# Kernel optimization log

Measured on AMD Instinct MI355X. Metric: run time of the kernel, lower is better.

The kernel has to match this reference:

```python
import jax, jax.numpy as jnp
import numpy as np

NUM_CLASSES = 10
OUTPUT_DIM = 128
HIDDEN_DIM = 64


def setup_inputs() -> dict:
    key = jax.random.key(0)
    k1, k2, k3, k4, k5, k6 = jax.random.split(key, 6)
    B, S, F = 16, 4096, 512
    X_support = jax.random.normal(k1, (B, S, F), dtype=jnp.float32)
    y_support = jax.random.randint(k2, (B, S), 0, NUM_CLASSES, dtype=jnp.int32)
    # MLP params: Linear(6, HIDDEN) -> GELU -> Linear(HIDDEN, OUTPUT)
    w1 = jax.random.normal(k3, (6, HIDDEN_DIM), dtype=jnp.float32) * (1.0 / np.sqrt(6.0))
    b1 = jax.random.normal(k4, (HIDDEN_DIM,), dtype=jnp.float32) * 0.01
    w2 = jax.random.normal(k5, (HIDDEN_DIM, OUTPUT_DIM), dtype=jnp.float32) * (1.0 / np.sqrt(HIDDEN_DIM))
    b2 = jax.random.normal(k6, (OUTPUT_DIM,), dtype=jnp.float32) * 0.01
    return {"X_support": X_support, "y_support": y_support,
            "w1": w1, "b1": b1, "w2": w2, "b2": b2}


def _feature_target_stats(X, y):
    """Vectorized equivalent of FeatureTargetStatsEncoder per-(batch,feature) loops.
    X: [B, S, F] float, y: [B, S] int class labels. Returns stats [B, F, 6]."""
    B, S, F = X.shape
    missing_rate = jnp.isnan(X).astype(X.dtype).mean(axis=1)           # [B, F]
    Xc = jnp.nan_to_num(X, nan=0.0)
    gmean = Xc.mean(axis=1)                                            # [B, F]
    variance = Xc.var(axis=1)                                          # biased (unbiased=False)
    absX = jnp.abs(Xc)
    mean_abs = absX.mean(axis=1)
    max_abs = absX.max(axis=1)
    # unique_ratio: count distinct values per (b, f) via sort + diff
    xs = jnp.sort(Xc, axis=1)
    n_unique = 1.0 + (jnp.diff(xs, axis=1) != 0).astype(Xc.dtype).sum(axis=1)
    unique_ratio = n_unique / S
    # classification target score: between-class variance / overall variance
    onehot = jax.nn.one_hot(y, NUM_CLASSES, dtype=Xc.dtype)            # [B, S, C]
    counts = onehot.sum(axis=1)                                        # [B, C]
    csum = jnp.einsum('bsc,bsf->bcf', onehot, Xc)                      # [B, C, F]
    cmean = csum / jnp.maximum(counts, 1.0)[:, :, None]
    dev2 = (cmean - gmean[:, None, :]) ** 2
    between = (counts[:, :, None] * dev2).sum(axis=1) / jnp.maximum(counts.sum(axis=1), 1.0)[:, None]
    target_score = between / jnp.maximum(variance, 1e-6)
    stats = jnp.stack([target_score, missing_rate, unique_ratio,
                       variance, mean_abs, max_abs], axis=-1)          # [B, F, 6]
    return jnp.nan_to_num(stats, nan=0.0, posinf=0.0, neginf=0.0)


def reference(X_support, y_support, w1, b1, w2, b2):
    stats = _feature_target_stats(X_support, y_support)                # [B, F, 6]
    h = jax.nn.gelu(stats @ w1 + b1, approximate=False)               # exact GELU like nn.GELU()
    return h @ w2 + b2                                                 # [B, F, OUTPUT_DIM]
```

## Files before the change

kernel.cpp:

```cpp
#include <hip/hip_runtime.h>
#include <math.h>

#define NS 4096
#define NF 512
#define NB 16
#define NC 10
#define HSIZE 8192
#define HMASK 8191
#define HEMPTY 0xFFFFFFFFu
#define WS_XT_OFF 1024

__global__ void count_classes_kernel(const int* __restrict__ y, float* __restrict__ counts) {
    __shared__ int hist[NC];
    const int b = blockIdx.x;
    if (threadIdx.x < NC) hist[threadIdx.x] = 0;
    __syncthreads();
    for (int s = threadIdx.x; s < NS; s += blockDim.x)
        atomicAdd(&hist[y[b * NS + s]], 1);
    __syncthreads();
    if (threadIdx.x < NC) counts[b * NC + threadIdx.x] = (float)hist[threadIdx.x];
}

__device__ __forceinline__ float wave_reduce_add(float v) {
    #pragma unroll
    for (int off = 32; off > 0; off >>= 1) v += __shfl_down(v, off, 64);
    return v;
}
__device__ __forceinline__ float wave_reduce_max(float v) {
    #pragma unroll
    for (int off = 32; off > 0; off >>= 1) v = fmaxf(v, __shfl_down(v, off, 64));
    return v;
}

__device__ __forceinline__ unsigned int pat_of(float x) {
    if (x != x) x = 0.f;
    unsigned int p = __float_as_uint(x);
    return (p == 0x80000000u) ? 0u : p;
}

__device__ __forceinline__ float resolve1(unsigned int* hash,
                                          unsigned int s, unsigned int p, unsigned int o) {
    if (o == HEMPTY) return 1.f;
    if (o == p)      return 0.f;
    for (;;) {
        s = (s + 1) & HMASK;
        const unsigned int oo = atomicCAS(&hash[s], HEMPTY, p);
        if (oo == HEMPTY) return 1.f;
        if (oo == p)      return 0.f;
    }
}

__device__ __forceinline__ float hash8(unsigned int* hash, const float4 u, const float4 v) {
    const unsigned int p0 = pat_of(u.x), p1 = pat_of(u.y), p2 = pat_of(u.z), p3 = pat_of(u.w);
    const unsigned int p4 = pat_of(v.x), p5 = pat_of(v.y), p6 = pat_of(v.z), p7 = pat_of(v.w);
    const unsigned int s0 = (p0 * 2654435761u) >> 19, s1 = (p1 * 2654435761u) >> 19;
    const unsigned int s2 = (p2 * 2654435761u) >> 19, s3 = (p3 * 2654435761u) >> 19;
    const unsigned int s4 = (p4 * 2654435761u) >> 19, s5 = (p5 * 2654435761u) >> 19;
    const unsigned int s6 = (p6 * 2654435761u) >> 19, s7 = (p7 * 2654435761u) >> 19;
    const unsigned int o0 = atomicCAS(&hash[s0], HEMPTY, p0);
    const unsigned int o1 = atomicCAS(&hash[s1], HEMPTY, p1);
    const unsigned int o2 = atomicCAS(&hash[s2], HEMPTY, p2);
    const unsigned int o3 = atomicCAS(&hash[s3], HEMPTY, p3);
    const unsigned int o4 = atomicCAS(&hash[s4], HEMPTY, p4);
    const unsigned int o5 = atomicCAS(&hash[s5], HEMPTY, p5);
    const unsigned int o6 = atomicCAS(&hash[s6], HEMPTY, p6);
    const unsigned int o7 = atomicCAS(&hash[s7], HEMPTY, p7);
    float u8 = 0.f;
    u8 += resolve1(hash, s0, p0, o0);
    u8 += resolve1(hash, s1, p1, o1);
    u8 += resolve1(hash, s2, p2, o2);
    u8 += resolve1(hash, s3, p3, o3);
    u8 += resolve1(hash, s4, p4, o4);
    u8 += resolve1(hash, s5, p5, o5);
    u8 += resolve1(hash, s6, p6, o6);
    u8 += resolve1(hash, s7, p7, o7);
    return u8;
}

__launch_bounds__(256)
__global__ void transpose_kernel(const float* __restrict__ X, float* __restrict__ XT,
                                 const int* __restrict__ y, float* __restrict__ counts) {
    __shared__ float t[64][65];
    __shared__ int hist[NC];
    const int b  = blockIdx.x;
    const int s0 = blockIdx.y * 64;
    const int f0 = blockIdx.z * 64;
    const int tid = threadIdx.x;

    const int fi = (tid & 15) * 4;
    const int si = tid >> 4;
    const float* Xb = X + ((size_t)b * NS + s0) * NF + f0;
    #pragma unroll
    for (int i = 0; i < 4; i++) {
        const int s = si + 16 * i;
        const float4 v = *(const float4*)(Xb + (size_t)s * NF + fi);
        t[s][fi + 0] = v.x; t[s][fi + 1] = v.y;
        t[s][fi + 2] = v.z; t[s][fi + 3] = v.w;
    }
    __syncthreads();

    const int sj = (tid & 15) * 4;
    const int fj = tid >> 4;
    float* XTb = XT + ((size_t)b * NF + f0) * NS + s0;
    #pragma unroll
    for (int i = 0; i < 4; i++) {
        const int f = fj + 16 * i;
        float4 v;
        v.x = t[sj + 0][f]; v.y = t[sj + 1][f];
        v.z = t[sj + 2][f]; v.w = t[sj + 3][f];
        *(float4*)(XTb + (size_t)f * NS + sj) = v;
    }

    if (blockIdx.y == 0 && blockIdx.z == 0) {
        if (tid < NC) hist[tid] = 0;
        __syncthreads();
        const int4* yb = (const int4*)(y + (size_t)b * NS);
        #pragma unroll
        for (int i = 0; i < 4; i++) {
            const int4 v = yb[i * 256 + tid];
            atomicAdd(&hist[v.x], 1); atomicAdd(&hist[v.y], 1);
            atomicAdd(&hist[v.z], 1); atomicAdd(&hist[v.w], 1);
        }
        __syncthreads();
        if (tid < NC) counts[b * NC + tid] = (float)hist[tid];
    }
}

__launch_bounds__(512, 8)
__global__ void fused_stats_mlp_xt(const float* __restrict__ XT,
                                   const int* __restrict__ y,
                                   const float* __restrict__ counts,
                                   const float* __restrict__ w1,
                                   const float* __restrict__ b1,
                                   const float* __restrict__ w2,
                                   const float* __restrict__ b2,
                                   float* __restrict__ out) {
    __shared__ __align__(16) unsigned int hash[HSIZE];

    const int w = blockIdx.x;
    const int g = (w & 7) * 1024 + (w >> 3);
    const int b = g >> 9;
    const int f = g & (NF - 1);
    const int tid = threadIdx.x;
    const int wave = tid >> 6;

    uint4* h4 = (uint4*)hash;
    const uint4 e4 = make_uint4(HEMPTY, HEMPTY, HEMPTY, HEMPTY);
    #pragma unroll
    for (int i = 0; i < HSIZE / 4 / 512; i++) h4[i * 512 + tid] = e4;
    __syncthreads();

    const float4* Xc4 = (const float4*)(XT + ((size_t)b * NF + f) * NS);
    const int4*   yp4 = (const int4*)(y + (size_t)b * NS);

    float sum = 0.f, sumsq = 0.f, sumabs = 0.f, maxabs = 0.f, nancnt = 0.f, uniq = 0.f;
    float csum[NC];
    #pragma unroll
    for (int c = 0; c < NC; c++) csum[c] = 0.f;

    if (wave < 4) {
        const int ts = tid;
        float4 xv[4]; int4 yv[4];
        #pragma unroll
        for (int k = 0; k < 4; k++) {
            xv[k] = Xc4[k * 256 + ts];
            yv[k] = yp4[k * 256 + ts];
        }
        #pragma unroll
        for (int k = 0; k < 4; k++) {
            const float xe[4] = { xv[k].x, xv[k].y, xv[k].z, xv[k].w };
            const int   ye[4] = { yv[k].x, yv[k].y, yv[k].z, yv[k].w };
            #pragma unroll
            for (int j = 0; j < 4; j++) {
                float x = xe[j];
                if (x != x) { nancnt += 1.f; x = 0.f; }
                sum += x;
                sumsq = fmaf(x, x, sumsq);
                const float a = fabsf(x);
                sumabs += a;
                maxabs = fmaxf(maxabs, a);
                const int yc = ye[j];
                #pragma unroll
                for (int c = 0; c < NC; c++) csum[c] += (yc == c) ? x : 0.f;
            }
        }
    } else {
        const int th = tid - 256;
        const float4 xa = Xc4[th];
        const float4 xb = Xc4[256 + th];
        const float4 xc = Xc4[512 + th];
        const float4 xd = Xc4[768 + th];
        uniq += hash8(hash, xa, xb);
        uniq += hash8(hash, xc, xd);
    }

    __syncthreads();

    float* r2 = (float*)hash;
    {
        float v16[16] = { sum, sumsq, sumabs, nancnt, uniq, maxabs,
                          csum[0], csum[1], csum[2], csum[3], csum[4],
                          csum[5], csum[6], csum[7], csum[8], csum[9] };
        #pragma unroll
        for (int c = 0; c < 16; c++) r2[c * 512 + tid] = v16[c];
    }
    __syncthreads();

    const int rc = tid >> 5;
    const int rq = tid & 31;
    float part = 0.f;
    #pragma unroll
    for (int j = 0; j < 16; j++) {
        const float v = r2[rc * 512 + rq + 32 * j];
        part = (rc == 5) ? fmaxf(part, v) : part + v;
    }
    #pragma unroll
    for (int off = 16; off > 0; off >>= 1) {
        const float o = __shfl_down(part, off, 32);
        part = (rc == 5) ? fmaxf(part, o) : part + o;
    }
    __syncthreads();
    if (rq == 0) r2[rc] = part;
    __syncthreads();

    float* stats_s = r2 + 32;
    float* h_s     = r2 + 64;

    if (tid == 0) {
        float t[16];
        #pragma unroll
        for (int v = 0; v < 16; v++) t[v] = r2[v];
        const float invS = 1.f / (float)NS;
        const float gmean    = t[0] * invS;
        const float variance = fmaxf(t[1] * invS - gmean * gmean, 0.f);
        const float mean_abs = t[2] * invS;
        const float missing  = t[3] * invS;
        const float n_unique = t[4];
        const float max_abs  = t[5];
        float between = 0.f;
        #pragma unroll
        for (int c = 0; c < NC; c++) {
            const float cnt = counts[b * NC + c];
            const float cm  = t[6 + c] / fmaxf(cnt, 1.f);
            const float d   = cm - gmean;
            between = fmaf(cnt * d, d, between);
        }
        between *= invS;
        const float target = between / fmaxf(variance, 1e-6f);
        float st[6] = { target, missing, n_unique * invS, variance, mean_abs, max_abs };
        #pragma unroll
        for (int i = 0; i < 6; i++) {
            float v = st[i];
            if (!(fabsf(v) < INFINITY)) v = 0.f;
            stats_s[i] = v;
        }
    }
    __syncthreads();

    if (tid < 64) {
        float z = b1[tid];
        #pragma unroll
        for (int i = 0; i < 6; i++) z = fmaf(stats_s[i], w1[i * 64 + tid], z);
        h_s[tid] = 0.5f * z * (1.f + erff(z * 0.70710678118654752440f));
    }
    __syncthreads();
    if (tid < 128) {
        float o = b2[tid];
        #pragma unroll
        for (int j = 0; j < 64; j++) o = fmaf(h_s[j], w2[j * 128 + tid], o);
        out[(size_t)g * 128 + tid] = o;
    }
}

__launch_bounds__(256)
__global__ void fused_stats_mlp_kernel(const float* __restrict__ X,
                                       const int* __restrict__ y,
                                       const float* __restrict__ counts,
                                       const float* __restrict__ w1,
                                       const float* __restrict__ b1,
                                       const float* __restrict__ w2,
                                       const float* __restrict__ b2,
                                       float* __restrict__ out) {
    __shared__ unsigned int hash[HSIZE];
    __shared__ float red[4][16];
    __shared__ float stats_s[6];
    __shared__ float h_s[64];

    const int w = blockIdx.x;
    const int g = (w & 7) * 1024 + (w >> 3);
    const int b = g >> 9;
    const int f = g & (NF - 1);
    const int tid = threadIdx.x;

    #pragma unroll
    for (int i = 0; i < HSIZE / 256; i++) hash[tid + i * 256] = HEMPTY;
    __syncthreads();

    const float* Xp = X + (size_t)b * NS * NF + f;
    const int*   yp = y + b * NS;

    float sum = 0.f, sumsq = 0.f, sumabs = 0.f, maxabs = 0.f, nancnt = 0.f, uniq = 0.f;
    float csum[NC];
    #pragma unroll
    for (int c = 0; c < NC; c++) csum[c] = 0.f;

    #pragma unroll
    for (int k0 = 0; k0 < 16; k0 += 8) {
        float xv[8]; int yv[8];
        #pragma unroll
        for (int k = 0; k < 8; k++) {
            const int s = (k0 + k) * 256 + tid;
            xv[k] = Xp[(size_t)s * NF];
            yv[k] = yp[s];
        }
        #pragma unroll
        for (int k = 0; k < 8; k++) {
            float x = xv[k];
            if (x != x) { nancnt += 1.f; x = 0.f; }
            sum += x;
            sumsq = fmaf(x, x, sumsq);
            const float a = fabsf(x);
            sumabs += a;
            maxabs = fmaxf(maxabs, a);
            const int yc = yv[k];
            #pragma unroll
            for (int c = 0; c < NC; c++) csum[c] += (yc == c) ? x : 0.f;
            unsigned int pat = __float_as_uint(x);
            if (pat == 0x80000000u) pat = 0u;
            unsigned int slot = (pat * 2654435761u) >> 19;
            for (;;) {
                const unsigned int old = atomicCAS(&hash[slot], HEMPTY, pat);
                if (old == HEMPTY) { uniq += 1.f; break; }
                if (old == pat) break;
                slot = (slot + 1) & HMASK;
            }
        }
    }

    sum    = wave_reduce_add(sum);
    sumsq  = wave_reduce_add(sumsq);
    sumabs = wave_reduce_add(sumabs);
    nancnt = wave_reduce_add(nancnt);
    uniq   = wave_reduce_add(uniq);
    maxabs = wave_reduce_max(maxabs);
    #pragma unroll
    for (int c = 0; c < NC; c++) csum[c] = wave_reduce_add(csum[c]);

    const int wave = tid >> 6, lane = tid & 63;
    if (lane == 0) {
        red[wave][0] = sum;    red[wave][1] = sumsq; red[wave][2] = sumabs;
        red[wave][3] = nancnt; red[wave][4] = uniq;  red[wave][5] = maxabs;
        #pragma unroll
        for (int c = 0; c < NC; c++) red[wave][6 + c] = csum[c];
    }
    __syncthreads();

    if (tid == 0) {
        float t[16];
        #pragma unroll
        for (int v = 0; v < 16; v++) t[v] = red[0][v];
        #pragma unroll
        for (int wv = 1; wv < 4; wv++) {
            #pragma unroll
            for (int v = 0; v < 16; v++) {
                if (v == 5) t[v] = fmaxf(t[v], red[wv][v]);
                else        t[v] += red[wv][v];
            }
        }
        const float invS = 1.f / (float)NS;
        const float gmean    = t[0] * invS;
        const float variance = fmaxf(t[1] * invS - gmean * gmean, 0.f);
        const float mean_abs = t[2] * invS;
        const float missing  = t[3] * invS;
        const float n_unique = t[4];
        const float max_abs  = t[5];
        float between = 0.f;
        #pragma unroll
        for (int c = 0; c < NC; c++) {
            const float cnt = counts[b * NC + c];
            const float cm  = t[6 + c] / fmaxf(cnt, 1.f);
            const float d   = cm - gmean;
            between += cnt * d * d;
        }
        between *= invS;
        const float target = between / fmaxf(variance, 1e-6f);
        float st[6] = { target, missing, n_unique * invS, variance, mean_abs, max_abs };
        #pragma unroll
        for (int i = 0; i < 6; i++) {
            float v = st[i];
            if (!(fabsf(v) < INFINITY)) v = 0.f;
            stats_s[i] = v;
        }
    }
    __syncthreads();

    if (tid < 64) {
        float z = b1[tid];
        #pragma unroll
        for (int i = 0; i < 6; i++) z = fmaf(stats_s[i], w1[i * 64 + tid], z);
        h_s[tid] = 0.5f * z * (1.f + erff(z * 0.70710678118654752440f));
    }
    __syncthreads();
    if (tid < 128) {
        float o = b2[tid];
        #pragma unroll
        for (int j = 0; j < 64; j++) o = fmaf(h_s[j], w2[j * 128 + tid], o);
        out[(size_t)g * 128 + tid] = o;
    }
}

extern "C" void kernel_launch(void* const* d_in, const int* in_sizes, int n_in,
                              void* d_out, int out_size, void* d_ws, size_t ws_size,
                              hipStream_t stream) {
    const float* X  = (const float*)d_in[0];
    const int*   y  = (const int*)d_in[1];
    const float* w1 = (const float*)d_in[2];
    const float* b1 = (const float*)d_in[3];
    const float* w2 = (const float*)d_in[4];
    const float* b2 = (const float*)d_in[5];
    float* out    = (float*)d_out;
    float* counts = (float*)d_ws;

    const size_t xt_bytes = (size_t)NB * NF * NS * sizeof(float);
    if (ws_size >= xt_bytes + WS_XT_OFF) {
        float* XT = (float*)((char*)d_ws + WS_XT_OFF);
        transpose_kernel<<<dim3(NB, NS / 64, NF / 64), 256, 0, stream>>>(X, XT, y, counts);
        fused_stats_mlp_xt<<<NB * NF, 512, 0, stream>>>(XT, y, counts, w1, b1, w2, b2, out);
    } else {
        count_classes_kernel<<<NB, 256, 0, stream>>>(y, counts);
        fused_stats_mlp_kernel<<<NB * NF, 256, 0, stream>>>(X, y, counts, w1, b1, w2, b2, out);
    }
}
```

Before: 348.6 us.

## Fuse moment and class-sum statistics into a striped transpose kernel

The transpose kernel now walks full sample columns in 16-feature stripes. While it writes the transposed copy, it also accumulates sum, sumsq, abs, max, NaN count and per-class sums, and stores the partials to a workspace buffer. The second kernel then only builds the hash for unique counting and runs the MLP, with all 512 threads doing hash work and no second reduction over moments. The grid shrinks to NB*NF/16 blocks with a serial loop over 32 sample tiles, which lowers parallelism in the transpose pass. The intent is to stop re-reading XT and y for the moments.

```diff
diff --git a/kernel.cpp b/kernel.cpp
--- a/kernel.cpp
+++ b/kernel.cpp
@@ -8,18 +8,10 @@
 #define HSIZE 8192
 #define HMASK 8191
 #define HEMPTY 0xFFFFFFFFu
-#define WS_XT_OFF 1024
-
-__global__ void count_classes_kernel(const int* __restrict__ y, float* __restrict__ counts) {
-    __shared__ int hist[NC];
-    const int b = blockIdx.x;
-    if (threadIdx.x < NC) hist[threadIdx.x] = 0;
-    __syncthreads();
-    for (int s = threadIdx.x; s < NS; s += blockDim.x)
-        atomicAdd(&hist[y[b * NS + s]], 1);
-    __syncthreads();
-    if (threadIdx.x < NC) counts[b * NC + threadIdx.x] = (float)hist[threadIdx.x];
-}
+#define TSR 128
+#define TSC 16
+#define WS_P_OFF  1024
+#define WS_XT_OFF (1024 + NB * NF * 16 * 4)
 
 __device__ __forceinline__ float wave_reduce_add(float v) {
     #pragma unroll
@@ -77,64 +69,103 @@
     return u8;
 }
 
-__launch_bounds__(256)
-__global__ void transpose_kernel(const float* __restrict__ X, float* __restrict__ XT,
-                                 const int* __restrict__ y, float* __restrict__ counts) {
-    __shared__ float t[64][65];
+__launch_bounds__(512, 4)
+__global__ void stripe_stats_kernel(const float* __restrict__ X,
+                                    float* __restrict__ XT,
+                                    const int* __restrict__ y,
+                                    float* __restrict__ P,
+                                    float* __restrict__ counts) {
+    __shared__ float t[TSR][TSC + 1];
+    __shared__ int ys[TSR];
     __shared__ int hist[NC];
-    const int b  = blockIdx.x;
-    const int s0 = blockIdx.y * 64;
-    const int f0 = blockIdx.z * 64;
+    const int b   = blockIdx.x;
+    const int f0  = blockIdx.y * TSC;
     const int tid = threadIdx.x;
-
-    const int fi = (tid & 15) * 4;
-    const int si = tid >> 4;
-    const float* Xb = X + ((size_t)b * NS + s0) * NF + f0;
-    #pragma unroll
-    for (int i = 0; i < 4; i++) {
-        const int s = si + 16 * i;
-        const float4 v = *(const float4*)(Xb + (size_t)s * NF + fi);
-        t[s][fi + 0] = v.x; t[s][fi + 1] = v.y;
-        t[s][fi + 2] = v.z; t[s][fi + 3] = v.w;
-    }
-    __syncthreads();
-
-    const int sj = (tid & 15) * 4;
-    const int fj = tid >> 4;
-    float* XTb = XT + ((size_t)b * NF + f0) * NS + s0;
-    #pragma unroll
-    for (int i = 0; i < 4; i++) {
-        const int f = fj + 16 * i;
-        float4 v;
-        v.x = t[sj + 0][f]; v.y = t[sj + 1][f];
-        v.z = t[sj + 2][f]; v.w = t[sj + 3][f];
-        *(float4*)(XTb + (size_t)f * NS + sj) = v;
-    }
-
-    if (blockIdx.y == 0 && blockIdx.z == 0) {
-        if (tid < NC) hist[tid] = 0;
+    const bool do_hist = (blockIdx.y == 0);
+    if (do_hist && tid < NC) hist[tid] = 0;
+
+    const int lrow = tid >> 2, lq = tid & 3;
+    const int col  = tid >> 5, rq = tid & 31;
+
+    const float* Xb = X + (size_t)b * NS * NF + f0 + lq * 4;
+    const int*   yb = y + (size_t)b * NS;
+
+    float sum = 0.f, sumsq = 0.f, sumabs = 0.f, maxabs = 0.f, nancnt = 0.f;
+    float csum[NC];
+    #pragma unroll
+    for (int c = 0; c < NC; c++) csum[c] = 0.f;
+
+    float4 xcur = *(const float4*)(Xb + (size_t)lrow * NF);
+    int4 ycur = make_int4(0, 0, 0, 0);
+    if (tid < TSR / 4) ycur = *(const int4*)(yb + tid * 4);
+
+    for (int it = 0; it < NS / TSR; ++it) {
+        const int s0 = it * TSR;
+        float4 xnext = xcur; int4 ynext = ycur;
+        if (it + 1 < NS / TSR) {
+            xnext = *(const float4*)(Xb + (size_t)(s0 + TSR + lrow) * NF);
+            if (tid < TSR / 4) ynext = *(const int4*)(yb + s0 + TSR + tid * 4);
+        }
         __syncthreads();
-        const int4* yb = (const int4*)(y + (size_t)b * NS);
-        #pragma unroll
-        for (int i = 0; i < 4; i++) {
-            const int4 v = yb[i * 256 + tid];
-            atomicAdd(&hist[v.x], 1); atomicAdd(&hist[v.y], 1);
-            atomicAdd(&hist[v.z], 1); atomicAdd(&hist[v.w], 1);
-        }
+        t[lrow][lq * 4 + 0] = xcur.x; t[lrow][lq * 4 + 1] = xcur.y;
+        t[lrow][lq * 4 + 2] = xcur.z; t[lrow][lq * 4 + 3] = xcur.w;
+        if (tid < TSR / 4) {
+            ys[tid * 4 + 0] = ycur.x; ys[tid * 4 + 1] = ycur.y;
+            ys[tid * 4 + 2] = ycur.z; ys[tid * 4 + 3] = ycur.w;
+        }
+        __syncthreads();
+        if (do_hist && tid < TSR) atomicAdd(&hist[ys[tid]], 1);
+
+        #pragma unroll
+        for (int j = 0; j < 4; j++) {
+            const int r = rq + 32 * j;
+            float x = t[r][col];
+            const int yc = ys[r];
+            if (x != x) { nancnt += 1.f; x = 0.f; }
+            sum += x;
+            sumsq = fmaf(x, x, sumsq);
+            const float a = fabsf(x);
+            sumabs += a;
+            maxabs = fmaxf(maxabs, a);
+            #pragma unroll
+            for (int c = 0; c < NC; c++) csum[c] += (yc == c) ? x : 0.f;
+        }
+        float4 wv;
+        wv.x = t[rq * 4 + 0][col]; wv.y = t[rq * 4 + 1][col];
+        wv.z = t[rq * 4 + 2][col]; wv.w = t[rq * 4 + 3][col];
+        *(float4*)(XT + ((size_t)b * NF + f0 + col) * NS + s0 + rq * 4) = wv;
+
+        xcur = xnext; ycur = ynext;
+    }
+
+    float st[16] = { sum, sumsq, sumabs, nancnt, maxabs,
+                     csum[0], csum[1], csum[2], csum[3], csum[4],
+                     csum[5], csum[6], csum[7], csum[8], csum[9], 0.f };
+    #pragma unroll
+    for (int s = 0; s < 15; s++) {
+        float v = st[s];
+        #pragma unroll
+        for (int off = 16; off > 0; off >>= 1) {
+            const float o = __shfl_down(v, off, 32);
+            v = (s == 4) ? fmaxf(v, o) : v + o;
+        }
+        if (rq == 0) P[((size_t)b * NF + f0 + col) * 16 + s] = v;
+    }
+    if (do_hist) {
         __syncthreads();
         if (tid < NC) counts[b * NC + tid] = (float)hist[tid];
     }
 }
 
 __launch_bounds__(512, 8)
-__global__ void fused_stats_mlp_xt(const float* __restrict__ XT,
-                                   const int* __restrict__ y,
-                                   const float* __restrict__ counts,
-                                   const float* __restrict__ w1,
-                                   const float* __restrict__ b1,
-                                   const float* __restrict__ w2,
-                                   const float* __restrict__ b2,
-                                   float* __restrict__ out) {
+__global__ void fused_hash_mlp(const float* __restrict__ XT,
+                               const float* __restrict__ P,
+                               const float* __restrict__ counts,
+                               const float* __restrict__ w1,
+                               const float* __restrict__ b1,
+                               const float* __restrict__ w2,
+                               const float* __restrict__ b2,
+                               float* __restrict__ out) {
     __shared__ __align__(16) unsigned int hash[HSIZE];
 
     const int w = blockIdx.x;
@@ -142,7 +173,7 @@
     const int b = g >> 9;
     const int f = g & (NF - 1);
     const int tid = threadIdx.x;
-    const int wave = tid >> 6;
+    const int wave = tid >> 6, lane = tid & 63;
 
     uint4* h4 = (uint4*)hash;
     const uint4 e4 = make_uint4(HEMPTY, HEMPTY, HEMPTY, HEMPTY);
@@ -151,106 +182,48 @@
     __syncthreads();
 
     const float4* Xc4 = (const float4*)(XT + ((size_t)b * NF + f) * NS);
-    const int4*   yp4 = (const int4*)(y + (size_t)b * NS);
-
-    float sum = 0.f, sumsq = 0.f, sumabs = 0.f, maxabs = 0.f, nancnt = 0.f, uniq = 0.f;
-    float csum[NC];
-    #pragma unroll
-    for (int c = 0; c < NC; c++) csum[c] = 0.f;
-
-    if (wave < 4) {
-        const int ts = tid;
-        float4 xv[4]; int4 yv[4];
-        #pragma unroll
-        for (int k = 0; k < 4; k++) {
-            xv[k] = Xc4[k * 256 + ts];
-            yv[k] = yp4[k * 256 + ts];
-        }
-        #pragma unroll
-        for (int k = 0; k < 4; k++) {
-            const float xe[4] = { xv[k].x, xv[k].y, xv[k].z, xv[k].w };
-            const int   ye[4] = { yv[k].x, yv[k].y, yv[k].z, yv[k].w };
-            #pragma unroll
-            for (int j = 0; j < 4; j++) {
-                float x = xe[j];
-                if (x != x) { nancnt += 1.f; x = 0.f; }
-                sum += x;
-                sumsq = fmaf(x, x, sumsq);
-                const float a = fabsf(x);
-                sumabs += a;
-                maxabs = fmaxf(maxabs, a);
-                const int yc = ye[j];
-                #pragma unroll
-                for (int c = 0; c < NC; c++) csum[c] += (yc == c) ? x : 0.f;
-            }
-        }
-    } else {
-        const int th = tid - 256;
-        const float4 xa = Xc4[th];
-        const float4 xb = Xc4[256 + th];
-        const float4 xc = Xc4[512 + th];
-        const float4 xd = Xc4[768 + th];
-        uniq += hash8(hash, xa, xb);
-        uniq += hash8(hash, xc, xd);
-    }
-
-    __syncthreads();
-
-    float* r2 = (float*)hash;
-    {
-        float v16[16] = { sum, sumsq, sumabs, nancnt, uniq, maxabs,
-                          csum[0], csum[1], csum[2], csum[3], csum[4],
-                          csum[5], csum[6], csum[7], csum[8], csum[9] };
-        #pragma unroll
-        for (int c = 0; c < 16; c++) r2[c * 512 + tid] = v16[c];
-    }
-    __syncthreads();
-
-    const int rc = tid >> 5;
-    const int rq = tid & 31;
-    float part = 0.f;
-    #pragma unroll
-    for (int j = 0; j < 16; j++) {
-        const float v = r2[rc * 512 + rq + 32 * j];
-        part = (rc == 5) ? fmaxf(part, v) : part + v;
-    }
-    #pragma unroll
-    for (int off = 16; off > 0; off >>= 1) {
-        const float o = __shfl_down(part, off, 32);
-        part = (rc == 5) ? fmaxf(part, o) : part + o;
-    }
-    __syncthreads();
-    if (rq == 0) r2[rc] = part;
-    __syncthreads();
-
-    float* stats_s = r2 + 32;
-    float* h_s     = r2 + 64;
+    const float4 xa = Xc4[tid];
+    const float4 xb = Xc4[512 + tid];
+    float uniq = hash8(hash, xa, xb);
+
+    __syncthreads();
+
+    float* r = (float*)hash;
+    float* stats_s = r + 32;
+    float* h_s = r + 64;
+
+    uniq = wave_reduce_add(uniq);
+    if (lane == 0) r[wave] = uniq;
+    __syncthreads();
 
     if (tid == 0) {
-        float t[16];
-        #pragma unroll
-        for (int v = 0; v < 16; v++) t[v] = r2[v];
+        float u = 0.f;
+        #pragma unroll
+        for (int i = 0; i < 8; i++) u += r[i];
+        const float* Pp = P + ((size_t)b * NF + f) * 16;
+        float S[15];
+        #pragma unroll
+        for (int s = 0; s < 15; s++) S[s] = Pp[s];
         const float invS = 1.f / (float)NS;
-        const float gmean    = t[0] * invS;
-        const float variance = fmaxf(t[1] * invS - gmean * gmean, 0.f);
-        const float mean_abs = t[2] * invS;
-        const float missing  = t[3] * invS;
-        const float n_unique = t[4];
-        const float max_abs  = t[5];
+        const float gmean    = S[0] * invS;
+        const float variance = fmaxf(S[1] * invS - gmean * gmean, 0.f);
+        const float mean_abs = S[2] * invS;
+        const float missing  = S[3] * invS;
+        const float max_abs  = S[4];
         float between = 0.f;
         #pragma unroll
         for (int c = 0; c < NC; c++) {
             const float cnt = counts[b * NC + c];
-            const float cm  = t[6 + c] / fmaxf(cnt, 1.f);
+            const float cm  = S[5 + c] / fmaxf(cnt, 1.f);
             const float d   = cm - gmean;
             between = fmaf(cnt * d, d, between);
         }
         between *= invS;
         const float target = between / fmaxf(variance, 1e-6f);
-        float st[6] = { target, missing, n_unique * invS, variance, mean_abs, max_abs };
+        float st6[6] = { target, missing, u * invS, variance, mean_abs, max_abs };
         #pragma unroll
         for (int i = 0; i < 6; i++) {
-            float v = st[i];
+            float v = st6[i];
             if (!(fabsf(v) < INFINITY)) v = 0.f;
             stats_s[i] = v;
         }
@@ -270,6 +243,17 @@
         for (int j = 0; j < 64; j++) o = fmaf(h_s[j], w2[j * 128 + tid], o);
         out[(size_t)g * 128 + tid] = o;
     }
+}
+
+__global__ void count_classes_kernel(const int* __restrict__ y, float* __restrict__ counts) {
+    __shared__ int hist[NC];
+    const int b = blockIdx.x;
+    if (threadIdx.x < NC) hist[threadIdx.x] = 0;
+    __syncthreads();
+    for (int s = threadIdx.x; s < NS; s += blockDim.x)
+        atomicAdd(&hist[y[b * NS + s]], 1);
+    __syncthreads();
+    if (threadIdx.x < NC) counts[b * NC + threadIdx.x] = (float)hist[threadIdx.x];
 }
 
 __launch_bounds__(256)
@@ -422,10 +406,11 @@
     float* counts = (float*)d_ws;
 
     const size_t xt_bytes = (size_t)NB * NF * NS * sizeof(float);
-    if (ws_size >= xt_bytes + WS_XT_OFF) {
+    if (ws_size >= (size_t)WS_XT_OFF + xt_bytes) {
+        float* P  = (float*)((char*)d_ws + WS_P_OFF);
         float* XT = (float*)((char*)d_ws + WS_XT_OFF);
-        transpose_kernel<<<dim3(NB, NS / 64, NF / 64), 256, 0, stream>>>(X, XT, y, counts);
-        fused_stats_mlp_xt<<<NB * NF, 512, 0, stream>>>(XT, y, counts, w1, b1, w2, b2, out);
+        stripe_stats_kernel<<<dim3(NB, NF / TSC), 512, 0, stream>>>(X, XT, y, P, counts);
+        fused_hash_mlp<<<NB * NF, 512, 0, stream>>>(XT, P, counts, w1, b1, w2, b2, out);
     } else {
         count_classes_kernel<<<NB, 256, 0, stream>>>(y, counts);
         fused_stats_mlp_kernel<<<NB * NF, 256, 0, stream>>>(X, y, counts, w1, b1, w2, b2, out);
```

New measurement: 325.8 us. 6.5% less time.
